# Performance work log

Hardware: AMD Instinct MI355X
Metric: run time of the kernel (lower is better)

## Reference

```python
import jax, jax.numpy as jnp
import numpy as np

N = 100000      # entity nodes
E = 1000000     # edges per relation
D_IN = 256
HID = 128
EPS = 1e-16     # PyG softmax denominator eps
NEG_SLOPE = 0.2 # GATConv default leaky_relu slope


def _gat_conv(x, ei, Ws, Wd, a_s, a_d, b):
    """Single-head GATConv (heads=1, concat=False) with self-loops."""
    n = x.shape[0]
    loop = jnp.arange(n, dtype=ei.dtype)
    src = jnp.concatenate([ei[0], loop])  # [E+N]
    dst = jnp.concatenate([ei[1], loop])
    h_src = x @ Ws                         # [N, HID]
    h_dst = x @ Wd                         # [N, HID]
    a_src = h_src @ a_s                    # [N]
    a_dst = h_dst @ a_d                    # [N]
    e = jax.nn.leaky_relu(a_src[src] + a_dst[dst], NEG_SLOPE)  # [E+N]
    # numerically-stable softmax over incoming edges of each dst node
    m = jax.ops.segment_max(e, dst, num_segments=n)
    ex = jnp.exp(e - m[dst])
    denom = jax.ops.segment_sum(ex, dst, num_segments=n)
    alpha = ex / (denom[dst] + EPS)        # [E+N]
    out = jax.ops.segment_sum(alpha[:, None] * h_src[src], dst, num_segments=n)
    return out + b


def setup_inputs() -> dict:
    key = jax.random.key(0)
    ks = jax.random.split(key, 9)
    s_in = 1.0 / np.sqrt(D_IN)
    s_h = 1.0 / np.sqrt(HID)
    return {
        "x": jax.random.normal(ks[0], (N, D_IN), dtype=jnp.float32),
        "edge_index_r0": jax.random.randint(ks[1], (2, E), 0, N, dtype=jnp.int64)
                         if jax.config.jax_enable_x64 else jax.random.randint(ks[1], (2, E), 0, N).astype(jnp.int32),
        "edge_index_r1": jax.random.randint(ks[2], (2, E), 0, N, dtype=jnp.int64)
                         if jax.config.jax_enable_x64 else jax.random.randint(ks[2], (2, E), 0, N).astype(jnp.int32),
        "W_src": jax.random.normal(ks[3], (2, D_IN, HID), dtype=jnp.float32) * s_in,
        "W_dst": jax.random.normal(ks[4], (2, D_IN, HID), dtype=jnp.float32) * s_in,
        "att_src": jax.random.normal(ks[5], (2, HID), dtype=jnp.float32) * s_h,
        "att_dst": jax.random.normal(ks[6], (2, HID), dtype=jnp.float32) * s_h,
        "bias": jnp.zeros((2, HID), dtype=jnp.float32),
    }


def reference(x, edge_index_r0, edge_index_r1, W_src, W_dst, att_src, att_dst, bias):
    # HeteroConv aggr='sum' over the two entity->entity relations
    out = _gat_conv(x, edge_index_r0, W_src[0], W_dst[0], att_src[0], att_dst[0], bias[0])
    out = out + _gat_conv(x, edge_index_r1, W_src[1], W_dst[1], att_src[1], att_dst[1], bias[1])
    # ELU; dropout p=0.0 is identity
    return jax.nn.elu(out)
```

## Files before the change

### kernel.cpp

```cpp
#include <hip/hip_runtime.h>

typedef __attribute__((ext_vector_type(8))) __bf16 bf16x8;
typedef __attribute__((ext_vector_type(4))) float floatx4;
typedef __attribute__((ext_vector_type(2))) float floatx2;

__device__ __forceinline__ float bf2f(unsigned short u) {
    return __uint_as_float(((unsigned)u) << 16);
}
__device__ __forceinline__ unsigned short f2bf(float f) {
    unsigned u = __float_as_uint(f);
    unsigned r = u + 0x7FFFu + ((u >> 16) & 1u);
    return (unsigned short)(r >> 16);
}

__global__ void detect_k(const unsigned short* __restrict__ xs, int* __restrict__ flag) {
    __shared__ int sred[256];
    int tid = threadIdx.x;
    int cnt = 0;
    for (int j = 0; j < 16; ++j) {
        unsigned short u = xs[(tid * 16 + j) * 2];
        int e = (u >> 7) & 0xFF;
        cnt += (e >= 96 && e <= 159) ? 1 : 0;
    }
    sred[tid] = cnt;
    __syncthreads();
    for (int s = 128; s > 0; s >>= 1) {
        if (tid < s) sred[tid] += sred[tid + s];
        __syncthreads();
    }
    if (tid == 0) *flag = (sred[0] > 2048) ? 1 : 0;
}

__device__ __forceinline__ void canon8(const void* src, unsigned short* dst,
                                       long long idx, int f) {
    if (f) {
        *(uint4*)&dst[idx] = *(const uint4*)((const unsigned short*)src + idx);
    } else {
        const float* sf = (const float*)src;
        unsigned short v[8];
        for (int j = 0; j < 8; ++j) v[j] = f2bf(sf[idx + j]);
        *(uint4*)&dst[idx] = *(const uint4*)v;
    }
}

__global__ void canon5_k(const void* Ws, const void* Wd, const void* as,
                         const void* ad, const void* b,
                         unsigned short* Wsb, unsigned short* Wdb,
                         unsigned short* asb, unsigned short* adb,
                         unsigned short* bsb, const int* __restrict__ flag) {
    int blk = blockIdx.x, tid = threadIdx.x;
    int f = *flag;
    if (blk < 64) {
        const void* src = blk < 32 ? Ws : Wd;
        unsigned short* dst = blk < 32 ? Wsb : Wdb;
        long long idx = ((long long)(blk & 31) * 256 + tid) * 8;
        canon8(src, dst, idx, f);
    } else {
        if (tid < 32)       canon8(as, asb, (long long)tid * 8, f);
        else if (tid < 64)  canon8(ad, adb, (long long)(tid - 32) * 8, f);
        else if (tid < 96)  canon8(b,  bsb, (long long)(tid - 64) * 8, f);
    }
}

__global__ void vec_kernel(const unsigned short* __restrict__ Ws,
                           const unsigned short* __restrict__ Wd,
                           const unsigned short* __restrict__ as_,
                           const unsigned short* __restrict__ ad_,
                           float* __restrict__ vecs) {
    int r = blockIdx.x;
    int k = threadIdx.x;
    float s = 0.f, t = 0.f;
    const unsigned short* wsrow = Ws + (size_t)r * 32768 + (size_t)k * 128;
    const unsigned short* wdrow = Wd + (size_t)r * 32768 + (size_t)k * 128;
    for (int h = 0; h < 128; ++h) {
        s += bf2f(wsrow[h]) * bf2f(as_[r * 128 + h]);
        t += bf2f(wdrow[h]) * bf2f(ad_[r * 128 + h]);
    }
    vecs[(r * 2 + 0) * 256 + k] = s;
    vecs[(r * 2 + 1) * 256 + k] = t;
}

__global__ void transpose_W(const unsigned short* __restrict__ W,
                            unsigned short* __restrict__ Bt) {
    int i = blockIdx.x * 256 + threadIdx.x;
    if (i >= 2 * 256 * 128) return;
    int r = i >> 15, rem = i & 32767;
    int k = rem >> 7, n = rem & 127;
    Bt[(size_t)r * 32768 + n * 256 + k] = W[i];
}

__global__ __launch_bounds__(256) void a_canon_k(const void* __restrict__ xraw,
                                                 unsigned short* __restrict__ xb,
                                                 const float* __restrict__ vecs,
                                                 float* __restrict__ aout, int n,
                                                 const int* __restrict__ flag) {
    __shared__ float sv[1024];
    int tid = threadIdx.x;
    for (int j = 0; j < 4; ++j) sv[j * 256 + tid] = vecs[j * 256 + tid];
    __syncthreads();
    int lane = tid & 63, wave = tid >> 6;
    int row = blockIdx.x * 4 + wave;
    if (row >= n) return;
    float xf[4];
    if (*flag) {
        uint2 u = *(const uint2*)((const unsigned short*)xraw + (size_t)row * 256 + lane * 4);
        xf[0] = bf2f((unsigned short)(u.x & 0xFFFF));
        xf[1] = bf2f((unsigned short)(u.x >> 16));
        xf[2] = bf2f((unsigned short)(u.y & 0xFFFF));
        xf[3] = bf2f((unsigned short)(u.y >> 16));
        *(uint2*)&xb[(size_t)row * 256 + lane * 4] = u;
    } else {
        float4 f = *(const float4*)((const float*)xraw + (size_t)row * 256 + lane * 4);
        xf[0] = f.x; xf[1] = f.y; xf[2] = f.z; xf[3] = f.w;
        unsigned short v[4] = {f2bf(f.x), f2bf(f.y), f2bf(f.z), f2bf(f.w)};
        *(uint2*)&xb[(size_t)row * 256 + lane * 4] = *(const uint2*)v;
    }
    float s[4] = {0.f, 0.f, 0.f, 0.f};
    for (int j = 0; j < 4; ++j)
        for (int q = 0; q < 4; ++q)
            s[j] += xf[q] * sv[j * 256 + lane * 4 + q];
    for (int j = 0; j < 4; ++j)
        for (int off = 32; off > 0; off >>= 1)
            s[j] += __shfl_down(s[j], off);
    if (lane == 0)
        for (int j = 0; j < 4; ++j) aout[(size_t)j * n + row] = s[j];
}

__device__ __forceinline__ void gload_lds16(const void* g, void* l) {
    __builtin_amdgcn_global_load_lds((const __attribute__((address_space(1))) void*)g,
                                     (__attribute__((address_space(3))) void*)l, 16, 0, 0);
}

__global__ __launch_bounds__(256) void gemm_h(const unsigned short* __restrict__ x,
                                              const unsigned short* __restrict__ Btg,
                                              unsigned short* __restrict__ hout, int n) {
    const int r = blockIdx.y;
    const unsigned short* bt = Btg + (size_t)r * 32768;
    unsigned short* h = hout + (size_t)r * n * 128;
    const int r0 = blockIdx.x * 128;
    __shared__ __align__(16) unsigned short As[128 * 64];
    __shared__ __align__(16) unsigned short Bs[128 * 64];
    int tid = threadIdx.x;
    int lane = tid & 63, wave = tid >> 6;
    int wm = wave >> 1, wn = wave & 1;

    floatx4 acc[4][4];
    for (int mt = 0; mt < 4; ++mt)
        for (int nt = 0; nt < 4; ++nt)
            acc[mt][nt] = (floatx4){0.f, 0.f, 0.f, 0.f};

    int srow = lane >> 3;
    int q    = lane & 7;
    int m16  = lane & 15;
    int qb   = lane >> 4;

    for (int k0 = 0; k0 < 256; k0 += 64) {
        for (int i = 0; i < 4; ++i) {
            int L = wave * 4 + i;
            int row = L * 8 + srow;
            int sw = ((q ^ (row & 7)) << 3);
            gload_lds16(x + (size_t)(r0 + row) * 256 + k0 + sw, &As[L * 512]);
            gload_lds16(bt + (size_t)row * 256 + k0 + sw, &Bs[L * 512]);
        }
        __syncthreads();
        for (int s = 0; s < 2; ++s) {
            int qr = qb + s * 4;
            bf16x8 af[4], bfv[4];
            for (int mt = 0; mt < 4; ++mt) {
                int row = wm * 64 + mt * 16 + m16;
                af[mt] = *(const bf16x8*)&As[row * 64 + ((qr ^ (row & 7)) << 3)];
            }
            for (int nt = 0; nt < 4; ++nt) {
                int row = wn * 64 + nt * 16 + m16;
                bfv[nt] = *(const bf16x8*)&Bs[row * 64 + ((qr ^ (row & 7)) << 3)];
            }
            for (int mt = 0; mt < 4; ++mt)
                for (int nt = 0; nt < 4; ++nt)
                    acc[mt][nt] = __builtin_amdgcn_mfma_f32_16x16x32_bf16(
                        af[mt], bfv[nt], acc[mt][nt], 0, 0, 0);
        }
        __syncthreads();
    }
    for (int mt = 0; mt < 4; ++mt) {
        int baser = r0 + wm * 64 + mt * 16 + qb * 4;
        for (int nt = 0; nt < 4; ++nt) {
            int c = wn * 64 + nt * 16 + m16;
            for (int i = 0; i < 4; ++i) {
                int gr = baser + i;
                if (gr < n) h[(size_t)gr * 128 + c] = f2bf(acc[mt][nt][i]);
            }
        }
    }
}

__global__ void hist2_k(const int* __restrict__ ei0, const int* __restrict__ ei1,
                        int* __restrict__ cnt0, int* __restrict__ cnt1,
                        int* __restrict__ rank0, int* __restrict__ rank1,
                        int E_, int n) {
    int rel = blockIdx.y;
    const int* ei = rel ? ei1 : ei0;
    int* cnt = rel ? cnt1 : cnt0;
    int* rank = rel ? rank1 : rank0;
    int t = blockIdx.x * 256 + threadIdx.x;
    if (t >= E_ + n) return;
    int d = (t < E_) ? ei[E_ + t] : (t - E_);
    rank[t] = atomicAdd(&cnt[d], 1);
}

__global__ __launch_bounds__(256) void scan_red_k(const int* __restrict__ cnt0,
                                                  const int* __restrict__ cnt1,
                                                  int* __restrict__ part,
                                                  int n, int nb) {
    __shared__ int s[256];
    int rel = blockIdx.y;
    const int* cnt = rel ? cnt1 : cnt0;
    int i = blockIdx.x * 256 + threadIdx.x;
    s[threadIdx.x] = (i < n) ? cnt[i] : 0;
    __syncthreads();
    for (int o = 128; o > 0; o >>= 1) {
        if (threadIdx.x < o) s[threadIdx.x] += s[threadIdx.x + o];
        __syncthreads();
    }
    if (threadIdx.x == 0) part[rel * nb + blockIdx.x] = s[0];
}

__global__ __launch_bounds__(1024) void scan_mid_k(int* __restrict__ part, int nb) {
    __shared__ int s[1024];
    int rel = blockIdx.x;
    int t = threadIdx.x;
    s[t] = (t < nb) ? part[rel * nb + t] : 0;
    __syncthreads();
    for (int o = 1; o < 1024; o <<= 1) {
        int v = (t >= o) ? s[t - o] : 0;
        __syncthreads();
        s[t] += v;
        __syncthreads();
    }
    if (t < nb) part[rel * nb + t] = (t == 0) ? 0 : s[t - 1];
}

__global__ __launch_bounds__(256) void scan_off_k(const int* __restrict__ cnt0,
                                                  const int* __restrict__ cnt1,
                                                  const int* __restrict__ part,
                                                  int* __restrict__ off0,
                                                  int* __restrict__ off1,
                                                  int n, int nb) {
    __shared__ int s[256];
    int rel = blockIdx.y;
    const int* cnt = rel ? cnt1 : cnt0;
    int* off = rel ? off1 : off0;
    int i = blockIdx.x * 256 + threadIdx.x;
    int t = threadIdx.x;
    int v = (i < n) ? cnt[i] : 0;
    s[t] = v;
    __syncthreads();
    for (int o = 1; o < 256; o <<= 1) {
        int u = (t >= o) ? s[t - o] : 0;
        __syncthreads();
        s[t] += u;
        __syncthreads();
    }
    if (i < n) off[i] = part[rel * nb + blockIdx.x] + s[t] - v;
}

__global__ void fill2_k(const int* __restrict__ ei0, const int* __restrict__ ei1,
                        const float* __restrict__ avals,
                        const int* __restrict__ off0, const int* __restrict__ off1,
                        const int* __restrict__ rank0, const int* __restrict__ rank1,
                        unsigned long long* __restrict__ pair0,
                        unsigned long long* __restrict__ pair1,
                        int E_, int n) {
    int rel = blockIdx.y;
    const int* ei = rel ? ei1 : ei0;
    const float* as_ = avals + (rel ? 2 * (size_t)n : 0);
    const float* ad_ = avals + (rel ? 3 * (size_t)n : (size_t)n);
    const int* off = rel ? off1 : off0;
    const int* rank = rel ? rank1 : rank0;
    unsigned long long* pair = rel ? pair1 : pair0;
    int t = blockIdx.x * 256 + threadIdx.x;
    if (t >= E_ + n) return;
    int s, d;
    if (t < E_) { s = ei[t]; d = ei[E_ + t]; } else { s = t - E_; d = s; }
    float e = as_[s] + ad_[d];
    e = e > 0.f ? e : 0.2f * e;
    float w = __expf(e);
    int pos = off[d] + rank[t];
    pair[pos] = ((unsigned long long)__float_as_uint(w) << 32) | (unsigned)s;
}

__device__ __forceinline__ void acc8pk(floatx2* a, float w, const uint4& hv) {
    floatx2 wv = {w, w};
    const unsigned u[4] = {hv.x, hv.y, hv.z, hv.w};
#pragma unroll
    for (int k = 0; k < 4; ++k) {
        floatx2 hf;
        hf.x = __uint_as_float(u[k] << 16);
        hf.y = __uint_as_float(u[k] & 0xFFFF0000u);
        asm("v_pk_fma_f32 %0, %1, %2, %0" : "+v"(a[k]) : "v"(wv), "v"(hf));
    }
}

__device__ __forceinline__ void rel_acc4(int d, int g, int l,
                                         const int* __restrict__ off,
                                         const int* __restrict__ cnt,
                                         const unsigned long long* __restrict__ pair,
                                         const unsigned short* __restrict__ h,
                                         float* __restrict__ o ) {
    int s0 = off[d];
    int e0 = s0 + cnt[d];
    float denom = 0.f;
    floatx2 a[4];
    a[0] = (floatx2){0.f, 0.f}; a[1] = (floatx2){0.f, 0.f};
    a[2] = (floatx2){0.f, 0.f}; a[3] = (floatx2){0.f, 0.f};
    int last = e0 - 1;
    for (int base = s0; base < e0; base += 8) {
        int i0 = base + g, i1 = i0 + 4;
        int j0 = min(i0, last), j1 = min(i1, last);
        unsigned long long p0 = pair[j0];
        unsigned long long p1 = pair[j1];
        uint4 hv0 = *(const uint4*)&h[(size_t)(unsigned)p0 * 128 + l * 8];
        uint4 hv1 = *(const uint4*)&h[(size_t)(unsigned)p1 * 128 + l * 8];
        float w0 = __uint_as_float((unsigned)(p0 >> 32));
        float w1 = __uint_as_float((unsigned)(p1 >> 32));
        w0 = (i0 <= last) ? w0 : 0.f;
        w1 = (i1 <= last) ? w1 : 0.f;
        denom += w0 + w1;
        acc8pk(a, w0, hv0);
        acc8pk(a, w1, hv1);
    }
    float t[8] = {a[0].x, a[0].y, a[1].x, a[1].y, a[2].x, a[2].y, a[3].x, a[3].y};
    for (int j = 0; j < 8; ++j) {
        t[j] += __shfl_xor(t[j], 16);
        t[j] += __shfl_xor(t[j], 32);
    }
    denom += __shfl_xor(denom, 16);
    denom += __shfl_xor(denom, 32);
    float inv = __builtin_amdgcn_rcpf(denom + 1e-16f);
    for (int j = 0; j < 8; ++j) o[j] = t[j] * inv;
}

__global__ __launch_bounds__(256) void agg_k(
    const int* __restrict__ off0, const int* __restrict__ cnt0,
    const unsigned long long* __restrict__ pair0,
    const int* __restrict__ off1, const int* __restrict__ cnt1,
    const unsigned long long* __restrict__ pair1,
    const unsigned short* __restrict__ h0, const unsigned short* __restrict__ h1,
    const unsigned short* __restrict__ bias, void* __restrict__ out,
    int n, const int* __restrict__ flag) {
    int wave = threadIdx.x >> 6, lane = threadIdx.x & 63;
    int g = lane >> 4, l = lane & 15;
    int d = blockIdx.x * 4 + wave;
    if (d >= n) return;
    float p[8], q[8];
    rel_acc4(d, g, l, off0, cnt0, pair0, h0, p);
    rel_acc4(d, g, l, off1, cnt1, pair1, h1, q);
    uint4 b0 = *(const uint4*)&bias[l * 8];
    uint4 b1 = *(const uint4*)&bias[128 + l * 8];
    const unsigned* b0u = (const unsigned*)&b0;
    const unsigned* b1u = (const unsigned*)&b1;
    float v[8];
    for (int j = 0; j < 8; ++j) {
        unsigned w0 = b0u[j >> 1], w1 = b1u[j >> 1];
        float bb = bf2f((unsigned short)((j & 1) ? (w0 >> 16) : (w0 & 0xFFFFu)))
                 + bf2f((unsigned short)((j & 1) ? (w1 >> 16) : (w1 & 0xFFFFu)));
        float t = p[j] + q[j] + bb;
        v[j] = t > 0.f ? t : (__expf(t) - 1.f);
    }
    if (g == 0) {
        if (*flag) {
            unsigned pk[4];
            for (int j = 0; j < 4; ++j)
                pk[j] = ((unsigned)f2bf(v[2 * j + 1]) << 16) | (unsigned)f2bf(v[2 * j]);
            ((uint4*)out)[(size_t)d * 16 + l] = *(const uint4*)pk;
        } else {
            float4 f0 = make_float4(v[0], v[1], v[2], v[3]);
            float4 f1 = make_float4(v[4], v[5], v[6], v[7]);
            ((float4*)out)[(size_t)d * 32 + l * 2] = f0;
            ((float4*)out)[(size_t)d * 32 + l * 2 + 1] = f1;
        }
    }
}

static inline char* carve(char*& p, size_t bytes) {
    char* r = p;
    p += (bytes + 255) & ~(size_t)255;
    return r;
}

extern "C" void kernel_launch(void* const* d_in, const int* in_sizes, int n_in,
                              void* d_out, int out_size, void* d_ws, size_t ws_size,
                              hipStream_t stream) {
    (void)n_in; (void)out_size; (void)ws_size;
    const void* x_raw  = d_in[0];
    const int*  ei0    = (const int*)d_in[1];
    const int*  ei1    = (const int*)d_in[2];
    const void* Ws_raw = d_in[3];
    const void* Wd_raw = d_in[4];
    const void* as_raw = d_in[5];
    const void* ad_raw = d_in[6];
    const void* b_raw  = d_in[7];

    const int n = in_sizes[0] / 256;
    const int e = in_sizes[1] / 2;
    const int tot = e + n;
    const int nb = (n + 255) / 256;

    char* p = (char*)d_ws;
    float* avals = (float*)carve(p, (size_t)4 * n * 4);
    int*   cnt0  = (int*)carve(p, (size_t)2 * n * 4);
    int*   cnt1  = cnt0 + n;
    int*   off0  = (int*)carve(p, (size_t)n * 4);
    int*   off1  = (int*)carve(p, (size_t)n * 4);
    int*   part  = (int*)carve(p, (size_t)2 * nb * 4);
    int*   rank0 = (int*)carve(p, (size_t)tot * 4);
    int*   rank1 = (int*)carve(p, (size_t)tot * 4);
    unsigned long long* pair0 = (unsigned long long*)carve(p, (size_t)tot * 8);
    unsigned long long* pair1 = (unsigned long long*)carve(p, (size_t)tot * 8);
    float* vecs  = (float*)carve(p, 1024 * 4);
    int*   flag  = (int*)carve(p, 256);
    unsigned short* xb  = (unsigned short*)carve(p, (size_t)(n + 128) * 256 * 2);
    unsigned short* h0  = (unsigned short*)carve(p, (size_t)2 * n * 128 * 2);
    unsigned short* h1  = h0 + (size_t)n * 128;
    unsigned short* Wsb = (unsigned short*)carve(p, 65536 * 2);
    unsigned short* Wdb = (unsigned short*)carve(p, 65536 * 2);
    unsigned short* Bt  = (unsigned short*)carve(p, 65536 * 2);
    unsigned short* asb = (unsigned short*)carve(p, 256 * 2);
    unsigned short* adb = (unsigned short*)carve(p, 256 * 2);
    unsigned short* bsb = (unsigned short*)carve(p, 256 * 2);

    hipMemsetAsync(cnt0, 0, (size_t)2 * n * 4, stream);

    detect_k<<<1, 256, 0, stream>>>((const unsigned short*)x_raw, flag);
    canon5_k<<<65, 256, 0, stream>>>(Ws_raw, Wd_raw, as_raw, ad_raw, b_raw,
                                     Wsb, Wdb, asb, adb, bsb, flag);
    vec_kernel<<<2, 256, 0, stream>>>(Wsb, Wdb, asb, adb, vecs);
    transpose_W<<<(2 * 256 * 128 + 255) / 256, 256, 0, stream>>>(Wsb, Bt);

    int gb = (tot + 255) / 256;
    hist2_k<<<dim3(gb, 2), 256, 0, stream>>>(ei0, ei1, cnt0, cnt1, rank0, rank1, e, n);
    scan_red_k<<<dim3(nb, 2), 256, 0, stream>>>(cnt0, cnt1, part, n, nb);
    scan_mid_k<<<2, 1024, 0, stream>>>(part, nb);
    scan_off_k<<<dim3(nb, 2), 256, 0, stream>>>(cnt0, cnt1, part, off0, off1, n, nb);

    a_canon_k<<<(n + 3) / 4, 256, 0, stream>>>(x_raw, xb, vecs, avals, n, flag);
    gemm_h<<<dim3((n + 127) / 128, 2), 256, 0, stream>>>(xb, Bt, h0, n);

    fill2_k<<<dim3(gb, 2), 256, 0, stream>>>(ei0, ei1, avals, off0, off1,
                                             rank0, rank1, pair0, pair1, e, n);

    agg_k<<<(n + 3) / 4, 256, 0, stream>>>(off0, cnt0, pair0, off1, cnt1, pair1,
                                           h0, h1, bsb, d_out, n, flag);
}
```

Baseline: 486.2 us.

## Fuse weight prep kernels and streamline aggregation loop with deferred reductions

Merges the weight canonicalization, attention-vector and transpose kernels into one prep kernel that reads raw weights directly, removing two launches and intermediate buffers. In the aggregation kernel, splits the edge loop into a branch-free full-chunk loop plus a tail, uses byte-offset addressing for h rows, and defers the cross-group shuffle reduction until after both relations are summed, halving the shuffles. The final normalization uses packed multiplies. Precision on the fp32 path changes slightly because the attention vectors are now computed from fp32 weights instead of bf16-rounded ones.

```diff
diff --git a/kernel.cpp b/kernel.cpp
--- a/kernel.cpp
+++ b/kernel.cpp
@@ -43,50 +43,49 @@
     }
 }
 
-__global__ void canon5_k(const void* Ws, const void* Wd, const void* as,
-                         const void* ad, const void* b,
-                         unsigned short* Wsb, unsigned short* Wdb,
-                         unsigned short* asb, unsigned short* adb,
-                         unsigned short* bsb, const int* __restrict__ flag) {
+__global__ void prep_k(const void* __restrict__ Ws, const void* __restrict__ Wd,
+                       const void* __restrict__ as, const void* __restrict__ ad,
+                       const void* __restrict__ b,
+                       unsigned short* __restrict__ Bt,
+                       unsigned short* __restrict__ bsb,
+                       float* __restrict__ vecs, const int* __restrict__ flag) {
     int blk = blockIdx.x, tid = threadIdx.x;
     int f = *flag;
-    if (blk < 64) {
-        const void* src = blk < 32 ? Ws : Wd;
-        unsigned short* dst = blk < 32 ? Wsb : Wdb;
-        long long idx = ((long long)(blk & 31) * 256 + tid) * 8;
-        canon8(src, dst, idx, f);
+    if (blk < 256) {
+        int i = blk * 256 + tid;
+        int r = i >> 15, rem = i & 32767;
+        int k = rem >> 7, nn = rem & 127;
+        unsigned short w = f ? ((const unsigned short*)Ws)[i]
+                             : f2bf(((const float*)Ws)[i]);
+        Bt[(size_t)r * 32768 + nn * 256 + k] = w;
+    } else if (blk < 258) {
+        int r = blk - 256;
+        int k = tid;
+        float s = 0.f, t = 0.f;
+        if (f) {
+            const unsigned short* wsrow = (const unsigned short*)Ws + (size_t)r * 32768 + (size_t)k * 128;
+            const unsigned short* wdrow = (const unsigned short*)Wd + (size_t)r * 32768 + (size_t)k * 128;
+            const unsigned short* asr = (const unsigned short*)as + r * 128;
+            const unsigned short* adr = (const unsigned short*)ad + r * 128;
+            for (int h = 0; h < 128; ++h) {
+                s += bf2f(wsrow[h]) * bf2f(asr[h]);
+                t += bf2f(wdrow[h]) * bf2f(adr[h]);
+            }
+        } else {
+            const float* wsrow = (const float*)Ws + (size_t)r * 32768 + (size_t)k * 128;
+            const float* wdrow = (const float*)Wd + (size_t)r * 32768 + (size_t)k * 128;
+            const float* asr = (const float*)as + r * 128;
+            const float* adr = (const float*)ad + r * 128;
+            for (int h = 0; h < 128; ++h) {
+                s += wsrow[h] * asr[h];
+                t += wdrow[h] * adr[h];
+            }
+        }
+        vecs[(r * 2 + 0) * 256 + k] = s;
+        vecs[(r * 2 + 1) * 256 + k] = t;
     } else {
-        if (tid < 32)       canon8(as, asb, (long long)tid * 8, f);
-        else if (tid < 64)  canon8(ad, adb, (long long)(tid - 32) * 8, f);
-        else if (tid < 96)  canon8(b,  bsb, (long long)(tid - 64) * 8, f);
-    }
-}
-
-__global__ void vec_kernel(const unsigned short* __restrict__ Ws,
-                           const unsigned short* __restrict__ Wd,
-                           const unsigned short* __restrict__ as_,
-                           const unsigned short* __restrict__ ad_,
-                           float* __restrict__ vecs) {
-    int r = blockIdx.x;
-    int k = threadIdx.x;
-    float s = 0.f, t = 0.f;
-    const unsigned short* wsrow = Ws + (size_t)r * 32768 + (size_t)k * 128;
-    const unsigned short* wdrow = Wd + (size_t)r * 32768 + (size_t)k * 128;
-    for (int h = 0; h < 128; ++h) {
-        s += bf2f(wsrow[h]) * bf2f(as_[r * 128 + h]);
-        t += bf2f(wdrow[h]) * bf2f(ad_[r * 128 + h]);
-    }
-    vecs[(r * 2 + 0) * 256 + k] = s;
-    vecs[(r * 2 + 1) * 256 + k] = t;
-}
-
-__global__ void transpose_W(const unsigned short* __restrict__ W,
-                            unsigned short* __restrict__ Bt) {
-    int i = blockIdx.x * 256 + threadIdx.x;
-    if (i >= 2 * 256 * 128) return;
-    int r = i >> 15, rem = i & 32767;
-    int k = rem >> 7, n = rem & 127;
-    Bt[(size_t)r * 32768 + n * 256 + k] = W[i];
+        if (tid < 32) canon8(b, bsb, (long long)tid * 8, f);
+    }
 }
 
 __global__ __launch_bounds__(256) void a_canon_k(const void* __restrict__ xraw,
@@ -300,26 +299,42 @@
     }
 }
 
-__device__ __forceinline__ void rel_acc4(int d, int g, int l,
+__device__ __forceinline__ void rel_acc4(int d, int g, unsigned l4,
                                          const int* __restrict__ off,
                                          const int* __restrict__ cnt,
                                          const unsigned long long* __restrict__ pair,
-                                         const unsigned short* __restrict__ h,
+                                         const char* __restrict__ h8,
                                          float* __restrict__ o ) {
     int s0 = off[d];
-    int e0 = s0 + cnt[d];
+    int deg = cnt[d];
+    int e0 = s0 + deg;
     float denom = 0.f;
     floatx2 a[4];
     a[0] = (floatx2){0.f, 0.f}; a[1] = (floatx2){0.f, 0.f};
     a[2] = (floatx2){0.f, 0.f}; a[3] = (floatx2){0.f, 0.f};
+    int base = s0;
+    int nfull = deg >> 3;
+    for (int it = 0; it < nfull; ++it, base += 8) {
+        int i0 = base + g, i1 = i0 + 4;
+        unsigned long long p0 = pair[i0];
+        unsigned long long p1 = pair[i1];
+        uint4 hv0 = *(const uint4*)(h8 + ((((unsigned)p0) << 8) + l4));
+        uint4 hv1 = *(const uint4*)(h8 + ((((unsigned)p1) << 8) + l4));
+        float w0 = __uint_as_float((unsigned)(p0 >> 32));
+        float w1 = __uint_as_float((unsigned)(p1 >> 32));
+        denom += w0 + w1;
+        acc8pk(a, w0, hv0);
+        acc8pk(a, w1, hv1);
+    }
+    int rem = e0 - base;
     int last = e0 - 1;
-    for (int base = s0; base < e0; base += 8) {
+    if (rem > 4) {
         int i0 = base + g, i1 = i0 + 4;
         int j0 = min(i0, last), j1 = min(i1, last);
         unsigned long long p0 = pair[j0];
         unsigned long long p1 = pair[j1];
-        uint4 hv0 = *(const uint4*)&h[(size_t)(unsigned)p0 * 128 + l * 8];
-        uint4 hv1 = *(const uint4*)&h[(size_t)(unsigned)p1 * 128 + l * 8];
+        uint4 hv0 = *(const uint4*)(h8 + ((((unsigned)p0) << 8) + l4));
+        uint4 hv1 = *(const uint4*)(h8 + ((((unsigned)p1) << 8) + l4));
         float w0 = __uint_as_float((unsigned)(p0 >> 32));
         float w1 = __uint_as_float((unsigned)(p1 >> 32));
         w0 = (i0 <= last) ? w0 : 0.f;
@@ -327,16 +342,25 @@
         denom += w0 + w1;
         acc8pk(a, w0, hv0);
         acc8pk(a, w1, hv1);
-    }
-    float t[8] = {a[0].x, a[0].y, a[1].x, a[1].y, a[2].x, a[2].y, a[3].x, a[3].y};
-    for (int j = 0; j < 8; ++j) {
-        t[j] += __shfl_xor(t[j], 16);
-        t[j] += __shfl_xor(t[j], 32);
+    } else if (rem > 0) {
+        int i0 = base + g;
+        int j0 = min(i0, last);
+        unsigned long long p0 = pair[j0];
+        uint4 hv0 = *(const uint4*)(h8 + ((((unsigned)p0) << 8) + l4));
+        float w0 = __uint_as_float((unsigned)(p0 >> 32));
+        w0 = (i0 <= last) ? w0 : 0.f;
+        denom += w0;
+        acc8pk(a, w0, hv0);
     }
     denom += __shfl_xor(denom, 16);
     denom += __shfl_xor(denom, 32);
     float inv = __builtin_amdgcn_rcpf(denom + 1e-16f);
-    for (int j = 0; j < 8; ++j) o[j] = t[j] * inv;
+    floatx2 iv = {inv, inv};
+#pragma unroll
+    for (int k = 0; k < 4; ++k)
+        asm("v_pk_mul_f32 %0, %0, %1" : "+v"(a[k]) : "v"(iv));
+    o[0] = a[0].x; o[1] = a[0].y; o[2] = a[1].x; o[3] = a[1].y;
+    o[4] = a[2].x; o[5] = a[2].y; o[6] = a[3].x; o[7] = a[3].y;
 }
 
 __global__ __launch_bounds__(256) void agg_k(
@@ -344,26 +368,30 @@
     const unsigned long long* __restrict__ pair0,
     const int* __restrict__ off1, const int* __restrict__ cnt1,
     const unsigned long long* __restrict__ pair1,
-    const unsigned short* __restrict__ h0, const unsigned short* __restrict__ h1,
+    const char* __restrict__ h0, const char* __restrict__ h1,
     const unsigned short* __restrict__ bias, void* __restrict__ out,
     int n, const int* __restrict__ flag) {
     int wave = threadIdx.x >> 6, lane = threadIdx.x & 63;
     int g = lane >> 4, l = lane & 15;
+    unsigned l4 = (unsigned)l << 4;
     int d = blockIdx.x * 4 + wave;
     if (d >= n) return;
     float p[8], q[8];
-    rel_acc4(d, g, l, off0, cnt0, pair0, h0, p);
-    rel_acc4(d, g, l, off1, cnt1, pair1, h1, q);
+    rel_acc4(d, g, l4, off0, cnt0, pair0, h0, p);
+    rel_acc4(d, g, l4, off1, cnt1, pair1, h1, q);
     uint4 b0 = *(const uint4*)&bias[l * 8];
     uint4 b1 = *(const uint4*)&bias[128 + l * 8];
     const unsigned* b0u = (const unsigned*)&b0;
     const unsigned* b1u = (const unsigned*)&b1;
     float v[8];
     for (int j = 0; j < 8; ++j) {
+        float s = p[j] + q[j];
+        s += __shfl_xor(s, 16);
+        s += __shfl_xor(s, 32);
         unsigned w0 = b0u[j >> 1], w1 = b1u[j >> 1];
         float bb = bf2f((unsigned short)((j & 1) ? (w0 >> 16) : (w0 & 0xFFFFu)))
                  + bf2f((unsigned short)((j & 1) ? (w1 >> 16) : (w1 & 0xFFFFu)));
-        float t = p[j] + q[j] + bb;
+        float t = s + bb;
         v[j] = t > 0.f ? t : (__expf(t) - 1.f);
     }
     if (g == 0) {
@@ -421,20 +449,14 @@
     unsigned short* xb  = (unsigned short*)carve(p, (size_t)(n + 128) * 256 * 2);
     unsigned short* h0  = (unsigned short*)carve(p, (size_t)2 * n * 128 * 2);
     unsigned short* h1  = h0 + (size_t)n * 128;
-    unsigned short* Wsb = (unsigned short*)carve(p, 65536 * 2);
-    unsigned short* Wdb = (unsigned short*)carve(p, 65536 * 2);
     unsigned short* Bt  = (unsigned short*)carve(p, 65536 * 2);
-    unsigned short* asb = (unsigned short*)carve(p, 256 * 2);
-    unsigned short* adb = (unsigned short*)carve(p, 256 * 2);
     unsigned short* bsb = (unsigned short*)carve(p, 256 * 2);
 
     hipMemsetAsync(cnt0, 0, (size_t)2 * n * 4, stream);
 
     detect_k<<<1, 256, 0, stream>>>((const unsigned short*)x_raw, flag);
-    canon5_k<<<65, 256, 0, stream>>>(Ws_raw, Wd_raw, as_raw, ad_raw, b_raw,
-                                     Wsb, Wdb, asb, adb, bsb, flag);
-    vec_kernel<<<2, 256, 0, stream>>>(Wsb, Wdb, asb, adb, vecs);
-    transpose_W<<<(2 * 256 * 128 + 255) / 256, 256, 0, stream>>>(Wsb, Bt);
+    prep_k<<<259, 256, 0, stream>>>(Ws_raw, Wd_raw, as_raw, ad_raw, b_raw,
+                                    Bt, bsb, vecs, flag);
 
     int gb = (tot + 255) / 256;
     hist2_k<<<dim3(gb, 2), 256, 0, stream>>>(ei0, ei1, cnt0, cnt1, rank0, rank1, e, n);
@@ -449,5 +471,6 @@
                                              rank0, rank1, pair0, pair1, e, n);
 
     agg_k<<<(n + 3) / 4, 256, 0, stream>>>(off0, cnt0, pair0, off1, cnt1, pair1,
-                                           h0, h1, bsb, d_out, n, flag);
-}
+                                           (const char*)h0, (const char*)h1,
+                                           bsb, d_out, n, flag);
+}
```

After: 469.4 us. -3.5%, faster.
